# Performance work log

Measured on AMD Instinct MI355X. Metric: run time of the kernel, lower is better.

Reference implementation:

```python
import jax, jax.numpy as jnp
import numpy as np

NEG_SLOPE = 0.2
EPS = 1e-16


def _gat_conv(x_src, x_dst, src, dst, W_src, W_dst, a_src, a_dst, b):
    """Single-head bipartite GAT-style conv (gather-score-softmax-scatter)."""
    num_dst = x_dst.shape[0]
    h_src = x_src @ W_src                      # [Ns, C]
    h_dst = x_dst @ W_dst                      # [Nd, C]
    s_src = h_src @ a_src                      # [Ns]
    s_dst = h_dst @ a_dst                      # [Nd]
    e = jax.nn.leaky_relu(s_src[src] + s_dst[dst], NEG_SLOPE)  # [E]
    # segment softmax over incoming edges of each dst node
    m = jax.ops.segment_max(e, dst, num_segments=num_dst)      # [Nd]
    w = jnp.exp(e - m[dst])
    denom = jax.ops.segment_sum(w, dst, num_segments=num_dst)  # [Nd]
    alpha = w / (denom[dst] + EPS)                             # [E]
    out = jax.ops.segment_sum(alpha[:, None] * h_src[src], dst, num_segments=num_dst)
    return out + b


def setup_inputs() -> dict:
    key = jax.random.key(0)
    ks = jax.random.split(key, 32)
    N_a, N_p, N_v = 100000, 150000, 10000
    F_in, C = 768, 64
    E_w, E_c, E_p = 300000, 1500000, 150000
    sc_in = 1.0 / np.sqrt(F_in)
    sc_c = 1.0 / np.sqrt(C)
    inp = {
        'x_author': jax.random.normal(ks[0], (N_a, F_in), jnp.float32),
        'x_paper': jax.random.normal(ks[1], (N_p, F_in), jnp.float32),
        'x_venue': jax.random.normal(ks[2], (N_v, F_in), jnp.float32),
        'writes_src': jax.random.randint(ks[3], (E_w,), 0, N_a, jnp.int32),
        'writes_dst': jax.random.randint(ks[4], (E_w,), 0, N_p, jnp.int32),
        'cites_src': jax.random.randint(ks[5], (E_c,), 0, N_p, jnp.int32),
        'cites_dst': jax.random.randint(ks[6], (E_c,), 0, N_p, jnp.int32),
        'pub_src': jax.random.randint(ks[7], (E_p,), 0, N_v, jnp.int32),
        'pub_dst': jax.random.randint(ks[8], (E_p,), 0, N_p, jnp.int32),
    }
    # per-edge-type learned params: W_src, W_dst [F_in, C], att vecs [C], bias [C]
    names = ['w', 'c', 'p']  # writes, cites, publishes
    for i, n in enumerate(names):
        base = 9 + 5 * i
        inp[f'W{n}_src'] = jax.random.normal(ks[base + 0], (F_in, C), jnp.float32) * sc_in
        inp[f'W{n}_dst'] = jax.random.normal(ks[base + 1], (F_in, C), jnp.float32) * sc_in
        inp[f'a{n}_src'] = jax.random.normal(ks[base + 2], (C,), jnp.float32) * sc_c
        inp[f'a{n}_dst'] = jax.random.normal(ks[base + 3], (C,), jnp.float32) * sc_c
        inp[f'b{n}'] = jnp.zeros((C,), jnp.float32)
    return inp


def reference(x_author, x_paper, x_venue,
              writes_src, writes_dst, cites_src, cites_dst, pub_src, pub_dst,
              Ww_src, Ww_dst, aw_src, aw_dst, bw,
              Wc_src, Wc_dst, ac_src, ac_dst, bc,
              Wp_src, Wp_dst, ap_src, ap_dst, bp):
    # HeteroConv with aggr='sum': all three edge types target 'paper'
    out_w = _gat_conv(x_author, x_paper, writes_src, writes_dst, Ww_src, Ww_dst, aw_src, aw_dst, bw)
    out_c = _gat_conv(x_paper, x_paper, cites_src, cites_dst, Wc_src, Wc_dst, ac_src, ac_dst, bc)
    out_p = _gat_conv(x_venue, x_paper, pub_src, pub_dst, Wp_src, Wp_dst, ap_src, ap_dst, bp)
    return out_w + out_c + out_p  # [N_paper, out_channels]
```

## Files before the change

### kernel.cpp

```cpp
#include <hip/hip_runtime.h>


#define F_IN 768
#define C_OUT 64
#define BN 80
#define TILE_M 64
#define BK 64
#define LDK 72
#define EPS 1e-16f

typedef __bf16 bf16x8 __attribute__((ext_vector_type(8)));
typedef float  f32x4  __attribute__((ext_vector_type(4)));

__global__ void prep_weights(
    const float* __restrict__ Ww_src, const float* __restrict__ aw_src,
    const float* __restrict__ Wc_src, const float* __restrict__ ac_src,
    const float* __restrict__ Wp_src, const float* __restrict__ ap_src,
    const float* __restrict__ Ww_dst, const float* __restrict__ aw_dst,
    const float* __restrict__ Wc_dst, const float* __restrict__ ac_dst,
    const float* __restrict__ Wp_dst, const float* __restrict__ ap_dst,
    __bf16* __restrict__ WTw, __bf16* __restrict__ WTc, __bf16* __restrict__ WTp)
{
    int type = blockIdx.x;
    const float* Ws = (type == 0) ? Ww_src : (type == 1) ? Wc_src : Wp_src;
    const float* as = (type == 0) ? aw_src : (type == 1) ? ac_src : ap_src;
    __bf16* WT = (type == 0) ? WTw : (type == 1) ? WTc : WTp;

    for (int r = threadIdx.x; r < F_IN; r += blockDim.x) {
        const float* wrow = Ws + (size_t)r * C_OUT;
        float u = 0.f;
        for (int c = 0; c < C_OUT; ++c) {
            float wv = wrow[c];
            WT[(size_t)c * F_IN + r] = (__bf16)wv;
            u += wv * as[c];
        }
        WT[(size_t)64 * F_IN + r] = (__bf16)u;
        for (int c = 65; c < BN; ++c) WT[(size_t)c * F_IN + r] = (__bf16)0.f;
        if (type == 1) {
            const float* r1 = Ww_dst + (size_t)r * C_OUT;
            const float* r2 = Wc_dst + (size_t)r * C_OUT;
            const float* r3 = Wp_dst + (size_t)r * C_OUT;
            float vw = 0.f, vc = 0.f, vp = 0.f;
            for (int c = 0; c < C_OUT; ++c) {
                vw += r1[c] * aw_dst[c];
                vc += r2[c] * ac_dst[c];
                vp += r3[c] * ap_dst[c];
            }
            WT[(size_t)65 * F_IN + r] = (__bf16)vw;
            WT[(size_t)66 * F_IN + r] = (__bf16)vc;
            WT[(size_t)67 * F_IN + r] = (__bf16)vp;
        }
    }
}

__global__ __launch_bounds__(256) void gemm_fused(
    const float* __restrict__ X, const __bf16* __restrict__ WT,
    float* __restrict__ H,
    float* __restrict__ s0, float* __restrict__ s1,
    float* __restrict__ s2, float* __restrict__ s3, int M)
{
    __shared__ __bf16 As[TILE_M][LDK];
    __shared__ __bf16 Bs[BN][LDK];

    const int tid  = threadIdx.x;
    const int lane = tid & 63;
    const int warp = tid >> 6;
    const int colq = lane & 15;
    const int quad = lane >> 4;
    const int rowBase = blockIdx.x * TILE_M;

    f32x4 acc[5];
#pragma unroll
    for (int t = 0; t < 5; ++t) acc[t] = (f32x4){0.f, 0.f, 0.f, 0.f};

    const int arow  = tid >> 2;
    const int akoff = (tid & 3) * 16;
    const int grow  = rowBase + arow;
    const bool rowOK = grow < M;
    const float* xrow = X + (size_t)grow * F_IN;

    for (int kc = 0; kc < F_IN; kc += BK) {
        f32x4 av[4];
        if (rowOK) {
            const f32x4* xp = (const f32x4*)(xrow + kc + akoff);
            av[0] = xp[0]; av[1] = xp[1]; av[2] = xp[2]; av[3] = xp[3];
        } else {
#pragma unroll
            for (int i = 0; i < 4; ++i) av[i] = (f32x4){0.f, 0.f, 0.f, 0.f};
        }
        bf16x8 cv[2];
#pragma unroll
        for (int i = 0; i < 4; ++i)
#pragma unroll
            for (int j = 0; j < 4; ++j)
                cv[i >> 1][(i & 1) * 4 + j] = (__bf16)av[i][j];
        *(bf16x8*)&As[arow][akoff]     = cv[0];
        *(bf16x8*)&As[arow][akoff + 8] = cv[1];

        for (int c = tid; c < (BN * BK / 8); c += 256) {
            int br = c >> 3, bo = (c & 7) * 8;
            *(bf16x8*)&Bs[br][bo] =
                *(const bf16x8*)&WT[(size_t)br * F_IN + kc + bo];
        }
        __syncthreads();

#pragma unroll
        for (int kk = 0; kk < BK; kk += 32) {
            bf16x8 a = *(const bf16x8*)&As[warp * 16 + colq][kk + quad * 8];
#pragma unroll
            for (int t = 0; t < 5; ++t) {
                bf16x8 b = *(const bf16x8*)&Bs[t * 16 + colq][kk + quad * 8];
                acc[t] = __builtin_amdgcn_mfma_f32_16x16x32_bf16(a, b, acc[t], 0, 0, 0);
            }
        }
        __syncthreads();
    }

    const int orow0 = rowBase + warp * 16 + quad * 4;
#pragma unroll
    for (int r = 0; r < 4; ++r) {
        int row = orow0 + r;
        if (row < M) {
#pragma unroll
            for (int t = 0; t < 4; ++t)
                H[(size_t)row * C_OUT + t * 16 + colq] = acc[t][r];
            if (colq < 4) {
                float* sp = (colq == 0) ? s0 : (colq == 1) ? s1 : (colq == 2) ? s2 : s3;
                if (sp) sp[row] = acc[4][r];
            }
        }
    }
}

__global__ void hist3(const int* __restrict__ d1, int E1,
                      const int* __restrict__ d2, int E2,
                      const int* __restrict__ d3, int E3,
                      int* __restrict__ cnt)
{
    int i0 = blockIdx.x * blockDim.x + threadIdx.x;
    int stride = gridDim.x * blockDim.x;
    for (int i = i0; i < E1; i += stride) atomicAdd(&cnt[d1[i]], 1);
    for (int i = i0; i < E2; i += stride) atomicAdd(&cnt[d2[i]], 1);
    for (int i = i0; i < E3; i += stride) atomicAdd(&cnt[d3[i]], 1);
}

__global__ void scan1(const int* __restrict__ cnt, int n,
                      int* __restrict__ rowptr, int* __restrict__ bsums)
{
    __shared__ int sm[256];
    const int t = threadIdx.x;
    const int base = blockIdx.x * 1024 + t * 4;
    int v[4];
    int tot = 0;
#pragma unroll
    for (int k = 0; k < 4; ++k) {
        v[k] = (base + k < n) ? cnt[base + k] : 0;
        tot += v[k];
    }
    sm[t] = tot;
    __syncthreads();
    for (int off = 1; off < 256; off <<= 1) {
        int add = (t >= off) ? sm[t - off] : 0;
        __syncthreads();
        sm[t] += add;
        __syncthreads();
    }
    int run = sm[t] - tot;
#pragma unroll
    for (int k = 0; k < 4; ++k) {
        if (base + k < n) rowptr[base + k] = run;
        run += v[k];
    }
    if (t == 255) bsums[blockIdx.x] = sm[255];
}

__global__ void scan2(int* __restrict__ bsums, int nb)
{
    __shared__ int sm[256];
    const int t = threadIdx.x;
    int v = (t < nb) ? bsums[t] : 0;
    sm[t] = v;
    __syncthreads();
    for (int off = 1; off < 256; off <<= 1) {
        int add = (t >= off) ? sm[t - off] : 0;
        __syncthreads();
        sm[t] += add;
        __syncthreads();
    }
    if (t < nb) bsums[t] = sm[t] - v;
}

__global__ void scan3(const int* __restrict__ bsums, int n, int Etot,
                      int* __restrict__ rowptr, int* __restrict__ cursor)
{
    int i = blockIdx.x * blockDim.x + threadIdx.x;
    if (i < n) {
        int r = rowptr[i] + bsums[i >> 10];
        rowptr[i] = r;
        cursor[i] = r;
    }
    if (i == 0) rowptr[n] = Etot;
}

__global__ void edge_sort3(const int* __restrict__ s1, const int* __restrict__ d1, int E1,
                           const int* __restrict__ s2, const int* __restrict__ d2, int E2,
                           const int* __restrict__ s3, const int* __restrict__ d3, int E3,
                           int* __restrict__ cursor, unsigned* __restrict__ eidx)
{
    int i0 = blockIdx.x * blockDim.x + threadIdx.x;
    int stride = gridDim.x * blockDim.x;
    for (int i = i0; i < E1; i += stride) {
        int p = atomicAdd(&cursor[d1[i]], 1);
        eidx[p] = (0u << 24) | (unsigned)s1[i];
    }
    for (int i = i0; i < E2; i += stride) {
        int p = atomicAdd(&cursor[d2[i]], 1);
        eidx[p] = (1u << 24) | (unsigned)s2[i];
    }
    for (int i = i0; i < E3; i += stride) {
        int p = atomicAdd(&cursor[d3[i]], 1);
        eidx[p] = (2u << 24) | (unsigned)s3[i];
    }
}

__global__ __launch_bounds__(256) void gat_gather(
    const unsigned* __restrict__ eidx, const int* __restrict__ rowptr,
    const float* __restrict__ Ha, const float* __restrict__ Hp, const float* __restrict__ Hv,
    const float* __restrict__ ssw, const float* __restrict__ ssc, const float* __restrict__ ssp,
    const float* __restrict__ sdw, const float* __restrict__ sdc, const float* __restrict__ sdp,
    const float* __restrict__ bw, const float* __restrict__ bc, const float* __restrict__ bp,
    float* __restrict__ out, int Nd)
{
    const int lane = threadIdx.x & 63;
    const int wid = (blockIdx.x * blockDim.x + threadIdx.x) >> 6;
    const int nw = (gridDim.x * blockDim.x) >> 6;
    const float bsum = bw[lane] + bc[lane] + bp[lane];

    for (int d = wid; d < Nd; d += nw) {
        const int start = rowptr[d];
        const int end   = rowptr[d + 1];
        const float sd0 = sdw[d], sd1 = sdc[d], sd2 = sdp[d];
        float a0 = 0.f, a1 = 0.f, a2 = 0.f;
        float dn0 = 0.f, dn1 = 0.f, dn2 = 0.f;

        for (int base = start; base < end; base += 64) {
            int n = end - base;
            if (n > 64) n = 64;
            unsigned ew = 0u;
            float w = 0.f;
            if (lane < n) {
                ew = eidx[base + lane];
                int t = (int)(ew >> 24);
                int s = (int)(ew & 0xFFFFFFu);
                float ss = (t == 0) ? ssw[s] : (t == 1) ? ssc[s] : ssp[s];
                float sd = (t == 0) ? sd0 : (t == 1) ? sd1 : sd2;
                float e = ss + sd;
                e = (e >= 0.f) ? e : 0.2f * e;
                w = __expf(e);
                if (t == 0) dn0 += w; else if (t == 1) dn1 += w; else dn2 += w;
            }
            int j = 0;
            for (; j + 4 <= n; j += 4) {
#pragma unroll
                for (int u = 0; u < 4; ++u) {
                    float wj = __shfl(w, j + u);
                    unsigned ej = (unsigned)__shfl((int)ew, j + u);
                    int tj = (int)(ej >> 24);
                    int sj = (int)(ej & 0xFFFFFFu);
                    const float* Hr = (tj == 0) ? Ha : (tj == 1) ? Hp : Hv;
                    float hv = Hr[(size_t)sj * C_OUT + lane];
                    if (tj == 0) a0 += wj * hv;
                    else if (tj == 1) a1 += wj * hv;
                    else a2 += wj * hv;
                }
            }
            for (; j < n; ++j) {
                float wj = __shfl(w, j);
                unsigned ej = (unsigned)__shfl((int)ew, j);
                int tj = (int)(ej >> 24);
                int sj = (int)(ej & 0xFFFFFFu);
                const float* Hr = (tj == 0) ? Ha : (tj == 1) ? Hp : Hv;
                float hv = Hr[(size_t)sj * C_OUT + lane];
                if (tj == 0) a0 += wj * hv;
                else if (tj == 1) a1 += wj * hv;
                else a2 += wj * hv;
            }
        }
#pragma unroll
        for (int off = 32; off > 0; off >>= 1) {
            dn0 += __shfl_xor(dn0, off);
            dn1 += __shfl_xor(dn1, off);
            dn2 += __shfl_xor(dn2, off);
        }
        out[(size_t)d * C_OUT + lane] =
            a0 / (dn0 + EPS) + a1 / (dn1 + EPS) + a2 / (dn2 + EPS) + bsum;
    }
}

extern "C" void kernel_launch(void* const* d_in, const int* in_sizes, int n_in,
                              void* d_out, int out_size, void* d_ws, size_t ws_size,
                              hipStream_t stream)
{
    const float* x_a = (const float*)d_in[0];
    const float* x_p = (const float*)d_in[1];
    const float* x_v = (const float*)d_in[2];
    const int* w_src = (const int*)d_in[3];
    const int* w_dst = (const int*)d_in[4];
    const int* c_src = (const int*)d_in[5];
    const int* c_dst = (const int*)d_in[6];
    const int* p_src = (const int*)d_in[7];
    const int* p_dst = (const int*)d_in[8];
    const float* Ww_src = (const float*)d_in[9];
    const float* Ww_dst = (const float*)d_in[10];
    const float* aw_src = (const float*)d_in[11];
    const float* aw_dst = (const float*)d_in[12];
    const float* bw     = (const float*)d_in[13];
    const float* Wc_src = (const float*)d_in[14];
    const float* Wc_dst = (const float*)d_in[15];
    const float* ac_src = (const float*)d_in[16];
    const float* ac_dst = (const float*)d_in[17];
    const float* bc     = (const float*)d_in[18];
    const float* Wp_src = (const float*)d_in[19];
    const float* Wp_dst = (const float*)d_in[20];
    const float* ap_src = (const float*)d_in[21];
    const float* ap_dst = (const float*)d_in[22];
    const float* bp     = (const float*)d_in[23];
    float* out = (float*)d_out;

    const int Na = in_sizes[0] / F_IN;
    const int Np = in_sizes[1] / F_IN;
    const int Nv = in_sizes[2] / F_IN;
    const int Ew = in_sizes[3];
    const int Ec = in_sizes[5];
    const int Ep = in_sizes[7];
    const int Etot = Ew + Ec + Ep;

    char* ws = (char*)d_ws;
    size_t off = 0;
    auto alloc = [&](size_t bytes) -> void* {
        off = (off + 255) & ~(size_t)255;
        void* p = ws + off;
        off += bytes;
        return p;
    };
    __bf16* WTw = (__bf16*)alloc((size_t)BN * F_IN * 2);
    __bf16* WTc = (__bf16*)alloc((size_t)BN * F_IN * 2);
    __bf16* WTp = (__bf16*)alloc((size_t)BN * F_IN * 2);
    float* Ha = (float*)alloc((size_t)Na * C_OUT * 4);
    float* Hp = (float*)alloc((size_t)Np * C_OUT * 4);
    float* Hv = (float*)alloc((size_t)Nv * C_OUT * 4);
    float* s_w_src = (float*)alloc((size_t)Na * 4);
    float* s_c_src = (float*)alloc((size_t)Np * 4);
    float* s_p_src = (float*)alloc((size_t)Nv * 4);
    float* s_w_dst = (float*)alloc((size_t)Np * 4);
    float* s_c_dst = (float*)alloc((size_t)Np * 4);
    float* s_p_dst = (float*)alloc((size_t)Np * 4);
    int* cnt    = (int*)alloc((size_t)Np * 4);
    int* rowptr = (int*)alloc((size_t)(Np + 1) * 4);
    int* cursor = (int*)alloc((size_t)Np * 4);
    int* bsums  = (int*)alloc(1024);
    unsigned* eidx = (unsigned*)alloc((size_t)Etot * 4);
    (void)ws_size; (void)n_in; (void)out_size;

    hipMemsetAsync(cnt, 0, (size_t)Np * 4, stream);

    prep_weights<<<3, 256, 0, stream>>>(
        Ww_src, aw_src, Wc_src, ac_src, Wp_src, ap_src,
        Ww_dst, aw_dst, Wc_dst, ac_dst, Wp_dst, ap_dst,
        WTw, WTc, WTp);

    gemm_fused<<<(Na + TILE_M - 1) / TILE_M, 256, 0, stream>>>(
        x_a, WTw, Ha, s_w_src, nullptr, nullptr, nullptr, Na);
    gemm_fused<<<(Np + TILE_M - 1) / TILE_M, 256, 0, stream>>>(
        x_p, WTc, Hp, s_c_src, s_w_dst, s_c_dst, s_p_dst, Np);
    gemm_fused<<<(Nv + TILE_M - 1) / TILE_M, 256, 0, stream>>>(
        x_v, WTp, Hv, s_p_src, nullptr, nullptr, nullptr, Nv);

    hist3<<<1024, 256, 0, stream>>>(w_dst, Ew, c_dst, Ec, p_dst, Ep, cnt);
    const int NB = (Np + 1023) / 1024;
    scan1<<<NB, 256, 0, stream>>>(cnt, Np, rowptr, bsums);
    scan2<<<1, 256, 0, stream>>>(bsums, NB);
    scan3<<<(Np + 255) / 256, 256, 0, stream>>>(bsums, Np, Etot, rowptr, cursor);
    edge_sort3<<<1024, 256, 0, stream>>>(
        w_src, w_dst, Ew, c_src, c_dst, Ec, p_src, p_dst, Ep, cursor, eidx);

    gat_gather<<<2048, 256, 0, stream>>>(
        eidx, rowptr, Ha, Hp, Hv,
        s_w_src, s_c_src, s_p_src, s_w_dst, s_c_dst, s_p_dst,
        bw, bc, bp, out, Np);
}
```

Measured before the change: 1.349 ms.

## Process four destination nodes per wavefront with 16-lane groups and float4 loads

The gather kernel now assigns each destination row to a 16-lane group instead of a full 64-lane wavefront. Each lane loads a float4 slice of the 64-channel source row, and edges are processed in chunks of 16 with group-local shuffles and reductions. The aim is to stop wasting lanes on low-degree nodes (about 13 incoming edges on average) and to issue wider loads. The cost is more divergence within a wave, because the four groups handle different nodes with different degrees.

Result: faster. 1.282 ms (-5.0%).

```diff
diff --git a/kernel.cpp b/kernel.cpp
--- a/kernel.cpp
+++ b/kernel.cpp
@@ -232,24 +232,34 @@
     float* __restrict__ out, int Nd)
 {
     const int lane = threadIdx.x & 63;
-    const int wid = (blockIdx.x * blockDim.x + threadIdx.x) >> 6;
-    const int nw = (gridDim.x * blockDim.x) >> 6;
-    const float bsum = bw[lane] + bc[lane] + bp[lane];
-
-    for (int d = wid; d < Nd; d += nw) {
+    const int q    = lane & 15;
+    const int gbase = lane & ~15;
+    const int gid  = (blockIdx.x * blockDim.x + threadIdx.x) >> 4;
+    const int ng   = (gridDim.x * blockDim.x) >> 4;
+
+    const f32x4* Ha4 = (const f32x4*)Ha;
+    const f32x4* Hp4 = (const f32x4*)Hp;
+    const f32x4* Hv4 = (const f32x4*)Hv;
+    f32x4* out4 = (f32x4*)out;
+
+    const f32x4 b4 = ((const f32x4*)bw)[q] + ((const f32x4*)bc)[q] + ((const f32x4*)bp)[q];
+
+    for (int d = gid; d < Nd; d += ng) {
         const int start = rowptr[d];
         const int end   = rowptr[d + 1];
         const float sd0 = sdw[d], sd1 = sdc[d], sd2 = sdp[d];
-        float a0 = 0.f, a1 = 0.f, a2 = 0.f;
+        f32x4 a0 = (f32x4){0.f,0.f,0.f,0.f};
+        f32x4 a1 = (f32x4){0.f,0.f,0.f,0.f};
+        f32x4 a2 = (f32x4){0.f,0.f,0.f,0.f};
         float dn0 = 0.f, dn1 = 0.f, dn2 = 0.f;
 
-        for (int base = start; base < end; base += 64) {
+        for (int base = start; base < end; base += 16) {
             int n = end - base;
-            if (n > 64) n = 64;
+            if (n > 16) n = 16;
             unsigned ew = 0u;
             float w = 0.f;
-            if (lane < n) {
-                ew = eidx[base + lane];
+            if (q < n) {
+                ew = eidx[base + q];
                 int t = (int)(ew >> 24);
                 int s = (int)(ew & 0xFFFFFFu);
                 float ss = (t == 0) ? ssw[s] : (t == 1) ? ssc[s] : ssp[s];
@@ -260,40 +270,40 @@
                 if (t == 0) dn0 += w; else if (t == 1) dn1 += w; else dn2 += w;
             }
             int j = 0;
-            for (; j + 4 <= n; j += 4) {
-#pragma unroll
-                for (int u = 0; u < 4; ++u) {
-                    float wj = __shfl(w, j + u);
-                    unsigned ej = (unsigned)__shfl((int)ew, j + u);
+            for (; j + 2 <= n; j += 2) {
+#pragma unroll
+                for (int u = 0; u < 2; ++u) {
+                    float wj = __shfl(w, gbase + j + u);
+                    unsigned ej = (unsigned)__shfl((int)ew, gbase + j + u);
                     int tj = (int)(ej >> 24);
                     int sj = (int)(ej & 0xFFFFFFu);
-                    const float* Hr = (tj == 0) ? Ha : (tj == 1) ? Hp : Hv;
-                    float hv = Hr[(size_t)sj * C_OUT + lane];
+                    const f32x4* Hr = (tj == 0) ? Ha4 : (tj == 1) ? Hp4 : Hv4;
+                    f32x4 hv = Hr[(size_t)sj * 16 + q];
                     if (tj == 0) a0 += wj * hv;
                     else if (tj == 1) a1 += wj * hv;
                     else a2 += wj * hv;
                 }
             }
             for (; j < n; ++j) {
-                float wj = __shfl(w, j);
-                unsigned ej = (unsigned)__shfl((int)ew, j);
+                float wj = __shfl(w, gbase + j);
+                unsigned ej = (unsigned)__shfl((int)ew, gbase + j);
                 int tj = (int)(ej >> 24);
                 int sj = (int)(ej & 0xFFFFFFu);
-                const float* Hr = (tj == 0) ? Ha : (tj == 1) ? Hp : Hv;
-                float hv = Hr[(size_t)sj * C_OUT + lane];
+                const f32x4* Hr = (tj == 0) ? Ha4 : (tj == 1) ? Hp4 : Hv4;
+                f32x4 hv = Hr[(size_t)sj * 16 + q];
                 if (tj == 0) a0 += wj * hv;
                 else if (tj == 1) a1 += wj * hv;
                 else a2 += wj * hv;
             }
         }
 #pragma unroll
-        for (int off = 32; off > 0; off >>= 1) {
+        for (int off = 8; off > 0; off >>= 1) {
             dn0 += __shfl_xor(dn0, off);
             dn1 += __shfl_xor(dn1, off);
             dn2 += __shfl_xor(dn2, off);
         }
-        out[(size_t)d * C_OUT + lane] =
-            a0 / (dn0 + EPS) + a1 / (dn1 + EPS) + a2 / (dn2 + EPS) + bsum;
+        f32x4 res = a0 / (dn0 + EPS) + a1 / (dn1 + EPS) + a2 / (dn2 + EPS) + b4;
+        out4[(size_t)d * 16 + q] = res;
     }
 }
 
```
